# Optimization experiments

Hardware: AMD Instinct MI355X
Metric: run time of the kernel (lower is better)

Reference implementation:

```python
import jax, jax.numpy as jnp
import numpy as np

K = 9          # kernel_size
CENTER = K // 2
EXTEND = 1.0   # extend_scope
B, C_IN, C_OUT, H, W = 2, 64, 64, 256, 256


def group_norm(x, w, b, groups, eps=1e-5):
    Bx, C, Hx, Wx = x.shape
    xg = x.reshape(Bx, groups, C // groups, Hx, Wx)
    m = xg.mean(axis=(2, 3, 4), keepdims=True)
    v = xg.var(axis=(2, 3, 4), keepdims=True)
    xn = ((xg - m) * jax.lax.rsqrt(v + eps)).reshape(Bx, C, Hx, Wx)
    return xn * w[None, :, None, None] + b[None, :, None, None]


def conv2d(x, w, b, stride, padding):
    y = jax.lax.conv_general_dilated(x, w, stride, padding,
                                     dimension_numbers=('NCHW', 'OIHW', 'NCHW'))
    return y + b[None, :, None, None]


def bilinear_sample(feat, iy, ix):
    # feat [B,C,H,W]; iy/ix pixel coords [B,Hg,Wg]; align_corners=True bilinear
    Hf, Wf = feat.shape[2], feat.shape[3]
    y0 = jnp.floor(iy); x0 = jnp.floor(ix)
    wy1 = iy - y0; wx1 = ix - x0
    wy0 = 1.0 - wy1; wx0 = 1.0 - wx1
    y0i = jnp.clip(y0, 0, Hf - 1).astype(jnp.int32)
    y1i = jnp.clip(y0 + 1, 0, Hf - 1).astype(jnp.int32)
    x0i = jnp.clip(x0, 0, Wf - 1).astype(jnp.int32)
    x1i = jnp.clip(x0 + 1, 0, Wf - 1).astype(jnp.int32)
    g = jax.vmap(lambda f, yi, xi: f[:, yi, xi])  # per-batch gather -> [B,C,Hg,Wg]
    return (g(feat, y0i, x0i) * (wy0 * wx0)[:, None]
            + g(feat, y0i, x1i) * (wy0 * wx1)[:, None]
            + g(feat, y1i, x0i) * (wy1 * wx0)[:, None]
            + g(feat, y1i, x1i) * (wy1 * wx1)[:, None])


def outward_cumsum(off):
    # off [B,K,H,W]: center row -> 0, cumulative sums outward from center
    lower = jnp.flip(jnp.cumsum(jnp.flip(off[:, :CENTER], axis=1), axis=1), axis=1)
    upper = jnp.cumsum(off[:, CENTER + 1:], axis=1)
    zero = jnp.zeros_like(off[:, :1])
    return jnp.concatenate([lower, zero, upper], axis=1)


def reference(x, w_off, b_off, gno_w, gno_b, w_dsc, b_dsc, gn_w, gn_b):
    Bx, _, Hx, Wx = x.shape
    # offset branch: conv3x3 -> GroupNorm(K, 2K) -> tanh
    offset = conv2d(x, w_off, b_off, (1, 1), ((1, 1), (1, 1)))
    offset = jnp.tanh(group_norm(offset, gno_w, gno_b, groups=K))
    y_off = offset[:, :K]                      # morph=0 uses the y half
    y_cum = outward_cumsum(y_off)              # [B,K,H,W]
    y_center = jnp.arange(Hx, dtype=x.dtype)[None, None, :, None]
    x_base = (jnp.arange(Wx, dtype=x.dtype)[None, None, None, :]
              + jnp.linspace(-CENTER, CENTER, K, dtype=x.dtype)[None, :, None, None])
    y_new = y_center + EXTEND * y_cum          # [B,K,H,W]
    x_new = jnp.broadcast_to(x_base, y_new.shape)
    # permute(0,2,1,3).reshape -> [B, K*H, W]
    ycoord = y_new.transpose(0, 2, 1, 3).reshape(Bx, Hx * K, Wx)
    xcoord = x_new.transpose(0, 2, 1, 3).reshape(Bx, Hx * K, Wx)
    # clamp to [0,max] then [-1,1] normalize + align_corners unnormalize == clamp
    iy = jnp.clip(ycoord, 0.0, Hx - 1.0)
    ix = jnp.clip(xcoord, 0.0, Wx - 1.0)
    deformed = bilinear_sample(x, iy, ix)      # [B,C,K*H,W]
    out = conv2d(deformed, w_dsc, b_dsc, (K, 1), 'VALID')  # [B,Cout,H,W]
    out = group_norm(out, gn_w, gn_b, groups=C_OUT // 4)
    return jax.nn.relu(out)


def setup_inputs() -> dict:
    key = jax.random.key(0)
    ks = jax.random.split(key, 3)
    return {
        'x': jax.random.normal(ks[0], (B, C_IN, H, W), dtype=jnp.float32),
        'w_off': jax.random.normal(ks[1], (2 * K, C_IN, 3, 3), dtype=jnp.float32) * 0.05,
        'b_off': jnp.zeros((2 * K,), dtype=jnp.float32),
        'gno_w': jnp.ones((2 * K,), dtype=jnp.float32),
        'gno_b': jnp.zeros((2 * K,), dtype=jnp.float32),
        'w_dsc': jax.random.normal(ks[2], (C_OUT, C_IN, K, 1), dtype=jnp.float32) * 0.05,
        'b_dsc': jnp.zeros((C_OUT,), dtype=jnp.float32),
        'gn_w': jnp.ones((C_OUT,), dtype=jnp.float32),
        'gn_b': jnp.zeros((C_OUT,), dtype=jnp.float32),
    }
```

## Files before the change

### kernel.cpp

```cpp
#include <hip/hip_runtime.h>
#include <hip/hip_fp16.h>
#include <math.h>

#define BB 2
#define CC 64
#define HH 256
#define WW 256
#define KK 9
#define NOFF 10
#define HW (HH*WW)

typedef __attribute__((ext_vector_type(8))) short s16x8;
typedef __attribute__((ext_vector_type(4))) float f32x4;

__device__ __forceinline__ unsigned lerp2h(unsigned a, unsigned b, __half2 fy2) {
    __half2 ah = *(__half2*)&a, bh = *(__half2*)&b;
    __half2 d = __hfma2(fy2, __hsub2(bh, ah), ah);
    return *(unsigned*)&d;
}

__global__ __launch_bounds__(256) void transpose_x_kernel(const float* __restrict__ x,
                                                          unsigned short* __restrict__ xTh) {
    __shared__ float tile[64 * 65];
    int wt = blockIdx.x & 3;
    int h  = (blockIdx.x >> 2) & 255;
    int b  = blockIdx.x >> 10;
    int w0 = wt * 64;
    int t  = threadIdx.x;
    {
        int wl = t & 63, crow = t >> 6;
        for (int it = 0; it < 16; ++it) {
            int c = crow + it * 4;
            tile[wl * 65 + c] = x[(((b * CC + c) * HH + h) * WW) + w0 + wl];
        }
    }
    __syncthreads();
    {
        int c2 = t & 31, wrow = t >> 5;
        unsigned* dst = (unsigned*)xTh;
        for (int it = 0; it < 8; ++it) {
            int wl = wrow + it * 8;
            __half2 p = __floats2half2_rn(tile[wl * 65 + c2 * 2], tile[wl * 65 + c2 * 2 + 1]);
            dst[(((b * HH + h) * WW) + w0 + wl) * 32 + c2] = *(unsigned*)&p;
        }
    }
}

__global__ __launch_bounds__(256) void pack_weights_kernel(const float* __restrict__ w_off,
                                                           const float* __restrict__ w_dsc,
                                                           unsigned short* __restrict__ woffB,
                                                           unsigned short* __restrict__ wdscB) {
    int idx = blockIdx.x * 256 + threadIdx.x;
    if (idx < 18 * 64 * 8) {
        int kb = idx >> 9;
        int L  = (idx >> 3) & 63;
        int j  = idx & 7;
        int n = L & 15, quad = L >> 4;
        int kk = kb * 32 + quad * 8 + j;
        int tap = kk >> 6, ci = kk & 63;
        float v = (n < NOFF) ? w_off[(n * 64 + ci) * 9 + tap] : 0.f;
        __half hv = __float2half(v);
        woffB[idx] = *(unsigned short*)&hv;
    }
    if (idx < 4 * 18 * 64 * 8) {
        int nt = idx / 9216;
        int r  = idx - nt * 9216;
        int kb = r >> 9;
        int L  = (r >> 3) & 63;
        int j  = r & 7;
        int n = L & 15, quad = L >> 4;
        int co = nt * 16 + n;
        int kk = kb * 32 + quad * 8 + j;
        int k = kk >> 6, ci = kk & 63;
        __half hv = __float2half(w_dsc[(co * 64 + ci) * 9 + k]);
        wdscB[idx] = *(unsigned short*)&hv;
    }
}

#define CPITCH 72
__global__ __launch_bounds__(256, 4) void conv_off_mfma(const unsigned short* __restrict__ xTh,
                                                        const unsigned short* __restrict__ woffB,
                                                        const float* __restrict__ b_off,
                                                        float* __restrict__ off_raw,
                                                        float* __restrict__ partials_off) {
    __shared__ unsigned short sx[3 * 66 * CPITCH];
    __shared__ float rs[4][16], rs2[4][16];
    int t = threadIdx.x;
    int L = t & 63, v = t >> 6;
    int b  = blockIdx.x >> 10;
    int h  = (blockIdx.x >> 2) & 255;
    int w0 = (blockIdx.x & 3) << 6;
    int col = L & 15, quad = L >> 4;

#pragma unroll
    for (int it = 0; it < 7; ++it) {
        int linear = it * 256 + t;
        if (linear < 1584) {
            int dy  = linear / 528;
            int rem = linear - dy * 528;
            int px  = rem >> 3, cg = rem & 7;
            int y  = h - 1 + dy;
            int xc = w0 - 1 + px;
            uint4 d = make_uint4(0, 0, 0, 0);
            if ((unsigned)y < 256u && (unsigned)xc < 256u)
                d = *(const uint4*)(xTh + ((size_t)(((b << 8) + y) << 8) + xc) * 64 + cg * 8);
            *(uint4*)&sx[(dy * 66 + px) * CPITCH + cg * 8] = d;
        }
    }

    s16x8 breg[18];
#pragma unroll
    for (int kb = 0; kb < 18; ++kb)
        breg[kb] = *(const s16x8*)(woffB + (kb * 64 + L) * 8);
    __syncthreads();

    f32x4 acc = {0.f, 0.f, 0.f, 0.f};
#pragma unroll
    for (int kb = 0; kb < 18; ++kb) {
        int tap = kb >> 1;
        int dy = tap / 3, dxl = tap % 3;
        int pxl = v * 16 + col + dxl;
        int ci0 = ((kb & 1) << 5) + quad * 8;
        s16x8 a = *(const s16x8*)&sx[(dy * 66 + pxl) * CPITCH + ci0];
        acc = __builtin_amdgcn_mfma_f32_16x16x32_f16(a, breg[kb], acc, 0, 0, 0);
    }
    int oc = col;
    float bo = b_off[oc];
    float s = 0.f, s2 = 0.f;
#pragma unroll
    for (int r = 0; r < 4; ++r) {
        float val = acc[r] + bo;
        if (oc < NOFF) {
            int w = w0 + v * 16 + quad * 4 + r;
            off_raw[((b * NOFF + oc) << 16) + (h << 8) + w] = val;
        }
        s += val; s2 += val * val;
    }
    s  += __shfl_xor(s, 16, 64);  s  += __shfl_xor(s, 32, 64);
    s2 += __shfl_xor(s2, 16, 64); s2 += __shfl_xor(s2, 32, 64);
    if (quad == 0) { rs[v][oc] = s; rs2[v][oc] = s2; }
    __syncthreads();
    if (t < NOFF) {
        float a_ = rs[0][t] + rs[1][t] + rs[2][t] + rs[3][t];
        float a2 = rs2[0][t] + rs2[1][t] + rs2[2][t] + rs2[3][t];
        partials_off[(size_t)blockIdx.x * 20 + t * 2]     = a_;
        partials_off[(size_t)blockIdx.x * 20 + t * 2 + 1] = a2;
    }
}

__global__ __launch_bounds__(256) void reduce_off_kernel(const float* __restrict__ partials,
                                                         float* __restrict__ stats) {
    int bg = blockIdx.x;
    int b = bg / 5, g = bg - b * 5;
    int t = threadIdx.x;
    float s = 0.f, s2 = 0.f;
    for (int i = t; i < 1024; i += 256) {
        const float* p = partials + ((size_t)(b * 1024 + i)) * 20 + g * 4;
        s  += p[0] + p[2];
        s2 += p[1] + p[3];
    }
    __shared__ float rs[256], rs2[256];
    rs[t] = s; rs2[t] = s2;
    __syncthreads();
    for (int o = 128; o > 0; o >>= 1) {
        if (t < o) { rs[t] += rs[t + o]; rs2[t] += rs2[t + o]; }
        __syncthreads();
    }
    if (t == 0) {
        float mean = rs[0] * (1.f / 131072.f);
        float var  = rs2[0] * (1.f / 131072.f) - mean * mean;
        stats[bg * 2]     = mean;
        stats[bg * 2 + 1] = rsqrtf(var + 1e-5f);
    }
}

__global__ __launch_bounds__(256) void reduce_out_kernel(const float* __restrict__ partials,
                                                         float* __restrict__ stats) {
    int bg = blockIdx.x;
    int b = bg >> 4, g = bg & 15;
    int t = threadIdx.x;
    float s = 0.f, s2 = 0.f;
    for (int i = t; i < 1024; i += 256) {
        const float* p = partials + ((size_t)(b * 1024 + i)) * 32 + g * 2;
        s  += p[0];
        s2 += p[1];
    }
    __shared__ float rs[256], rs2[256];
    rs[t] = s; rs2[t] = s2;
    __syncthreads();
    for (int o = 128; o > 0; o >>= 1) {
        if (t < o) { rs[t] += rs[t + o]; rs2[t] += rs2[t + o]; }
        __syncthreads();
    }
    if (t == 0) {
        float mean = rs[0] * (1.f / 262144.f);
        float var  = rs2[0] * (1.f / 262144.f) - mean * mean;
        stats[bg * 2]     = mean;
        stats[bg * 2 + 1] = rsqrtf(var + 1e-5f);
    }
}

__global__ __launch_bounds__(256, 4) void main_mfma(const unsigned short* __restrict__ xTh,
                                                    const float* __restrict__ off_raw,
                                                    const float* __restrict__ stats_off,
                                                    const float* __restrict__ gno_w,
                                                    const float* __restrict__ gno_b,
                                                    const unsigned short* __restrict__ wdscB,
                                                    const float* __restrict__ b_dsc,
                                                    unsigned short* __restrict__ tmph,
                                                    float* __restrict__ partials_out) {
    __shared__ unsigned short aT[32 * 584];
    __shared__ int            offA0[576];
    __shared__ unsigned short fyH[576];

    int t = threadIdx.x;
    int L = t & 63, nt = t >> 6;
    int b  = blockIdx.x >> 10;
    int h  = (blockIdx.x >> 2) & 255;
    int w0 = (blockIdx.x & 3) << 6;

    if (t < 64) {
        int w = w0 + t;
        float tk[9];
#pragma unroll
        for (int k = 0; k < 9; ++k) {
            float vv = off_raw[((b * NOFF + k) << 16) + (h << 8) + w];
            int g = k >> 1;
            float mean = stats_off[(b * 5 + g) * 2];
            float rstd = stats_off[(b * 5 + g) * 2 + 1];
            tk[k] = tanhf((vv - mean) * rstd * gno_w[k] + gno_b[k]);
        }
        float yc[9];
        float c = 0.f;
#pragma unroll
        for (int k = 3; k >= 0; --k) { c += tk[k]; yc[k] = c; }
        yc[4] = 0.f;
        c = 0.f;
#pragma unroll
        for (int k = 5; k < 9; ++k) { c += tk[k]; yc[k] = c; }
#pragma unroll
        for (int k = 0; k < 9; ++k) {
            float y = fminf(fmaxf((float)h + yc[k], 0.f), 255.f);
            float y0f = floorf(y);
            int y0 = (int)y0f;
            int xc = min(max(w + k - 4, 0), 255);
            offA0[t * 9 + k] = ((b * 256 + y0) * 256 + xc) * 64;
            __half fh = __float2half(y - y0f);
            fyH[t * 9 + k] = *(unsigned short*)&fh;
        }
    }

    s16x8 wreg[18];
#pragma unroll
    for (int kb = 0; kb < 18; ++kb)
        wreg[kb] = *(const s16x8*)(wdscB + ((nt * 18 + kb) * 64 + L) * 8);

    int col = L & 15, quad = L >> 4;
    int co = nt * 16 + col;
    float bias = b_dsc[co];
    float ss = 0.f, ss2 = 0.f;

    for (int round = 0; round < 2; ++round) {
        __syncthreads();
#pragma unroll
        for (int it = 0; it < 9; ++it) {
            int idx = it * 256 + t;
            int cg  = idx & 7;
            int r2  = idx >> 3;
            int pxl = r2 / 9;
            int k   = r2 - pxl * 9;
            int pi  = (round * 32 + pxl) * 9 + k;
            int o0 = offA0[pi] + cg * 8;
            unsigned short fb = fyH[pi];
            int o1 = fb ? o0 + 16384 : o0;
            __half fh = *(__half*)&fb;
            __half2 fy2 = __half2half2(fh);
            uint4 u0 = *(const uint4*)(xTh + o0);
            uint4 u1 = *(const uint4*)(xTh + o1);
            uint4 d;
            d.x = lerp2h(u0.x, u1.x, fy2);
            d.y = lerp2h(u0.y, u1.y, fy2);
            d.z = lerp2h(u0.z, u1.z, fy2);
            d.w = lerp2h(u0.w, u1.w, fy2);
            int c2 = (cg + k) & 7;
            *(uint4*)&aT[pxl * 584 + k * 64 + c2 * 8] = d;
        }
        __syncthreads();

#pragma unroll
        for (int sub = 0; sub < 2; ++sub) {
            int row = sub * 16 + col;
            f32x4 acc = {0.f, 0.f, 0.f, 0.f};
#pragma unroll
            for (int kb = 0; kb < 18; ++kb) {
                int k  = kb >> 1;
                int cch = ((kb & 1) << 2) + quad;
                int c2 = (cch + k) & 7;
                s16x8 a = *(const s16x8*)&aT[row * 584 + k * 64 + c2 * 8];
                acc = __builtin_amdgcn_mfma_f32_16x16x32_f16(a, wreg[kb], acc, 0, 0, 0);
            }
            int wbase = w0 + round * 32 + sub * 16 + quad * 4;
            size_t obase = ((size_t)((b << 16) + (h << 8) + wbase)) * 64 + co;
#pragma unroll
            for (int r = 0; r < 4; ++r) {
                float val = acc[r] + bias;
                ss += val; ss2 += val * val;
                __half hv = __float2half(val);
                tmph[obase + (size_t)r * 64] = *(unsigned short*)&hv;
            }
        }
    }
    ss  += __shfl_xor(ss, 16, 64);  ss  += __shfl_xor(ss, 32, 64);
    ss2 += __shfl_xor(ss2, 16, 64); ss2 += __shfl_xor(ss2, 32, 64);
    float sg = ss, sg2 = ss2;
    sg  += __shfl_xor(sg, 1, 64);  sg  += __shfl_xor(sg, 2, 64);
    sg2 += __shfl_xor(sg2, 1, 64); sg2 += __shfl_xor(sg2, 2, 64);
    if (quad == 0 && (col & 3) == 0) {
        int gi = nt * 4 + (col >> 2);
        partials_out[(size_t)blockIdx.x * 32 + gi * 2]     = sg;
        partials_out[(size_t)blockIdx.x * 32 + gi * 2 + 1] = sg2;
    }
}

__global__ __launch_bounds__(256) void apply_final_kernel(const unsigned short* __restrict__ tmph,
                                                          const float* __restrict__ stats_out,
                                                          const float* __restrict__ gn_w,
                                                          const float* __restrict__ gn_b,
                                                          float* __restrict__ out) {
    __shared__ float tile[64 * 65];
    int wt = blockIdx.x & 3;
    int h  = (blockIdx.x >> 2) & 255;
    int b  = blockIdx.x >> 10;
    int w0 = wt * 64;
    int t  = threadIdx.x;
    {
        int c2 = t & 31, wrow = t >> 5;
        int co0 = c2 * 2;
        int g = co0 >> 2;
        float mean = stats_out[(b * 16 + g) * 2];
        float rstd = stats_out[(b * 16 + g) * 2 + 1];
        float sc0 = rstd * gn_w[co0],     sh0 = gn_b[co0]     - mean * sc0;
        float sc1 = rstd * gn_w[co0 + 1], sh1 = gn_b[co0 + 1] - mean * sc1;
        const unsigned* src = (const unsigned*)tmph;
        for (int it = 0; it < 8; ++it) {
            int wl = wrow + it * 8;
            unsigned u = src[(((b * HH + h) * WW) + w0 + wl) * 32 + c2];
            float2 f = __half22float2(*(__half2*)&u);
            tile[co0 * 65 + wl]       = fmaxf(fmaf(f.x, sc0, sh0), 0.f);
            tile[(co0 + 1) * 65 + wl] = fmaxf(fmaf(f.y, sc1, sh1), 0.f);
        }
    }
    __syncthreads();
    {
        int wl = t & 63, crow = t >> 6;
        for (int it = 0; it < 16; ++it) {
            int co = crow + it * 4;
            out[((size_t)(b * CC + co) * HH + h) * WW + w0 + wl] = tile[co * 65 + wl];
        }
    }
}

extern "C" void kernel_launch(void* const* d_in, const int* in_sizes, int n_in,
                              void* d_out, int out_size, void* d_ws, size_t ws_size,
                              hipStream_t stream) {
    const float* x     = (const float*)d_in[0];
    const float* w_off = (const float*)d_in[1];
    const float* b_off = (const float*)d_in[2];
    const float* gno_w = (const float*)d_in[3];
    const float* gno_b = (const float*)d_in[4];
    const float* w_dsc = (const float*)d_in[5];
    const float* b_dsc = (const float*)d_in[6];
    const float* gn_w  = (const float*)d_in[7];
    const float* gn_b  = (const float*)d_in[8];
    float* out = (float*)d_out;

    char* ws = (char*)d_ws;
    unsigned short* xTh   = (unsigned short*)(ws);
    unsigned short* tmph  = (unsigned short*)(ws + 16777216);
    float* off_raw        = (float*)(ws + 33554432);
    unsigned short* wdscB = (unsigned short*)(ws + 38797312);
    unsigned short* woffB = (unsigned short*)(ws + 38871040);
    float* stats_off      = (float*)(ws + 38889472);
    float* stats_out      = (float*)(ws + 38889728);
    float* partials_off   = (float*)(ws + 38890496);
    float* partials_out   = (float*)(ws + 39054336);

    hipLaunchKernelGGL(transpose_x_kernel, dim3(2048), dim3(256), 0, stream, x, xTh);
    hipLaunchKernelGGL(pack_weights_kernel, dim3(144), dim3(256), 0, stream,
                       w_off, w_dsc, woffB, wdscB);
    hipLaunchKernelGGL(conv_off_mfma, dim3(2048), dim3(256), 0, stream,
                       xTh, woffB, b_off, off_raw, partials_off);
    hipLaunchKernelGGL(reduce_off_kernel, dim3(10), dim3(256), 0, stream,
                       partials_off, stats_off);
    hipLaunchKernelGGL(main_mfma, dim3(2048), dim3(256), 0, stream,
                       xTh, off_raw, stats_off, gno_w, gno_b, wdscB, b_dsc,
                       tmph, partials_out);
    hipLaunchKernelGGL(reduce_out_kernel, dim3(32), dim3(256), 0, stream,
                       partials_out, stats_out);
    hipLaunchKernelGGL(apply_final_kernel, dim3(2048), dim3(256), 0, stream,
                       tmph, stats_out, gn_w, gn_b, out);
}
```

Baseline: 163.7 us.

## Merge weight packing into transpose, shrink main tile, parallelize offset tanh

Folds the weight-packing kernel into the transpose kernel as extra blocks, removing one launch. In main_mfma, the LDS A-tile is halved (16 pixels per round, 4 rounds) and launch bounds are raised to 6 waves/EU to increase occupancy. The tanh/GroupNorm offset computation is spread across all 256 threads via a shared buffer instead of only 64 threads. The weight register loads are moved ahead of the barrier to overlap with it. The cost is more barriers per block and possible register pressure under the tighter launch bound.

```diff
diff --git a/kernel.cpp b/kernel.cpp
--- a/kernel.cpp
+++ b/kernel.cpp
@@ -20,7 +20,39 @@
 }
 
 __global__ __launch_bounds__(256) void transpose_x_kernel(const float* __restrict__ x,
-                                                          unsigned short* __restrict__ xTh) {
+                                                          unsigned short* __restrict__ xTh,
+                                                          const float* __restrict__ w_off,
+                                                          const float* __restrict__ w_dsc,
+                                                          unsigned short* __restrict__ woffB,
+                                                          unsigned short* __restrict__ wdscB) {
+    if (blockIdx.x >= 2048) {
+        int idx = (blockIdx.x - 2048) * 256 + threadIdx.x;
+        if (idx < 18 * 64 * 8) {
+            int kb = idx >> 9;
+            int L  = (idx >> 3) & 63;
+            int j  = idx & 7;
+            int n = L & 15, quad = L >> 4;
+            int kk = kb * 32 + quad * 8 + j;
+            int tap = kk >> 6, ci = kk & 63;
+            float v = (n < NOFF) ? w_off[(n * 64 + ci) * 9 + tap] : 0.f;
+            __half hv = __float2half(v);
+            woffB[idx] = *(unsigned short*)&hv;
+        }
+        if (idx < 4 * 18 * 64 * 8) {
+            int nt = idx / 9216;
+            int r  = idx - nt * 9216;
+            int kb = r >> 9;
+            int L  = (r >> 3) & 63;
+            int j  = r & 7;
+            int n = L & 15, quad = L >> 4;
+            int co = nt * 16 + n;
+            int kk = kb * 32 + quad * 8 + j;
+            int k = kk >> 6, ci = kk & 63;
+            __half hv = __float2half(w_dsc[(co * 64 + ci) * 9 + k]);
+            wdscB[idx] = *(unsigned short*)&hv;
+        }
+        return;
+    }
     __shared__ float tile[64 * 65];
     int wt = blockIdx.x & 3;
     int h  = (blockIdx.x >> 2) & 255;
@@ -43,37 +75,6 @@
             __half2 p = __floats2half2_rn(tile[wl * 65 + c2 * 2], tile[wl * 65 + c2 * 2 + 1]);
             dst[(((b * HH + h) * WW) + w0 + wl) * 32 + c2] = *(unsigned*)&p;
         }
-    }
-}
-
-__global__ __launch_bounds__(256) void pack_weights_kernel(const float* __restrict__ w_off,
-                                                           const float* __restrict__ w_dsc,
-                                                           unsigned short* __restrict__ woffB,
-                                                           unsigned short* __restrict__ wdscB) {
-    int idx = blockIdx.x * 256 + threadIdx.x;
-    if (idx < 18 * 64 * 8) {
-        int kb = idx >> 9;
-        int L  = (idx >> 3) & 63;
-        int j  = idx & 7;
-        int n = L & 15, quad = L >> 4;
-        int kk = kb * 32 + quad * 8 + j;
-        int tap = kk >> 6, ci = kk & 63;
-        float v = (n < NOFF) ? w_off[(n * 64 + ci) * 9 + tap] : 0.f;
-        __half hv = __float2half(v);
-        woffB[idx] = *(unsigned short*)&hv;
-    }
-    if (idx < 4 * 18 * 64 * 8) {
-        int nt = idx / 9216;
-        int r  = idx - nt * 9216;
-        int kb = r >> 9;
-        int L  = (r >> 3) & 63;
-        int j  = r & 7;
-        int n = L & 15, quad = L >> 4;
-        int co = nt * 16 + n;
-        int kk = kb * 32 + quad * 8 + j;
-        int k = kk >> 6, ci = kk & 63;
-        __half hv = __float2half(w_dsc[(co * 64 + ci) * 9 + k]);
-        wdscB[idx] = *(unsigned short*)&hv;
     }
 }
 
@@ -200,7 +201,7 @@
     }
 }
 
-__global__ __launch_bounds__(256, 4) void main_mfma(const unsigned short* __restrict__ xTh,
+__global__ __launch_bounds__(256, 6) void main_mfma(const unsigned short* __restrict__ xTh,
                                                     const float* __restrict__ off_raw,
                                                     const float* __restrict__ stats_off,
                                                     const float* __restrict__ gno_w,
@@ -209,9 +210,10 @@
                                                     const float* __restrict__ b_dsc,
                                                     unsigned short* __restrict__ tmph,
                                                     float* __restrict__ partials_out) {
-    __shared__ unsigned short aT[32 * 584];
+    __shared__ unsigned short aT[16 * 584];
     __shared__ int            offA0[576];
     __shared__ unsigned short fyH[576];
+    __shared__ float          tkL[576];
 
     int t = threadIdx.x;
     int L = t & 63, nt = t >> 6;
@@ -219,17 +221,27 @@
     int h  = (blockIdx.x >> 2) & 255;
     int w0 = (blockIdx.x & 3) << 6;
 
+    for (int i = t; i < 576; i += 256) {
+        int k = i >> 6, w = i & 63;
+        float vv = off_raw[((b * NOFF + k) << 16) + (h << 8) + w0 + w];
+        int g = k >> 1;
+        float mean = stats_off[(b * 5 + g) * 2];
+        float rstd = stats_off[(b * 5 + g) * 2 + 1];
+        tkL[w * 9 + k] = tanhf((vv - mean) * rstd * gno_w[k] + gno_b[k]);
+    }
+
+    s16x8 wreg[18];
+#pragma unroll
+    for (int kb = 0; kb < 18; ++kb)
+        wreg[kb] = *(const s16x8*)(wdscB + ((nt * 18 + kb) * 64 + L) * 8);
+
+    __syncthreads();
+
     if (t < 64) {
         int w = w0 + t;
         float tk[9];
 #pragma unroll
-        for (int k = 0; k < 9; ++k) {
-            float vv = off_raw[((b * NOFF + k) << 16) + (h << 8) + w];
-            int g = k >> 1;
-            float mean = stats_off[(b * 5 + g) * 2];
-            float rstd = stats_off[(b * 5 + g) * 2 + 1];
-            tk[k] = tanhf((vv - mean) * rstd * gno_w[k] + gno_b[k]);
-        }
+        for (int k = 0; k < 9; ++k) tk[k] = tkL[t * 9 + k];
         float yc[9];
         float c = 0.f;
 #pragma unroll
@@ -250,26 +262,19 @@
         }
     }
 
-    s16x8 wreg[18];
-#pragma unroll
-    for (int kb = 0; kb < 18; ++kb)
-        wreg[kb] = *(const s16x8*)(wdscB + ((nt * 18 + kb) * 64 + L) * 8);
-
     int col = L & 15, quad = L >> 4;
     int co = nt * 16 + col;
     float bias = b_dsc[co];
     float ss = 0.f, ss2 = 0.f;
 
-    for (int round = 0; round < 2; ++round) {
+    for (int round = 0; round < 4; ++round) {
         __syncthreads();
-#pragma unroll
-        for (int it = 0; it < 9; ++it) {
-            int idx = it * 256 + t;
+        for (int idx = t; idx < 1152; idx += 256) {
             int cg  = idx & 7;
             int r2  = idx >> 3;
             int pxl = r2 / 9;
             int k   = r2 - pxl * 9;
-            int pi  = (round * 32 + pxl) * 9 + k;
+            int pi  = (round * 16 + pxl) * 9 + k;
             int o0 = offA0[pi] + cg * 8;
             unsigned short fb = fyH[pi];
             int o1 = fb ? o0 + 16384 : o0;
@@ -287,27 +292,23 @@
         }
         __syncthreads();
 
-#pragma unroll
-        for (int sub = 0; sub < 2; ++sub) {
-            int row = sub * 16 + col;
-            f32x4 acc = {0.f, 0.f, 0.f, 0.f};
-#pragma unroll
-            for (int kb = 0; kb < 18; ++kb) {
-                int k  = kb >> 1;
-                int cch = ((kb & 1) << 2) + quad;
-                int c2 = (cch + k) & 7;
-                s16x8 a = *(const s16x8*)&aT[row * 584 + k * 64 + c2 * 8];
-                acc = __builtin_amdgcn_mfma_f32_16x16x32_f16(a, wreg[kb], acc, 0, 0, 0);
-            }
-            int wbase = w0 + round * 32 + sub * 16 + quad * 4;
-            size_t obase = ((size_t)((b << 16) + (h << 8) + wbase)) * 64 + co;
-#pragma unroll
-            for (int r = 0; r < 4; ++r) {
-                float val = acc[r] + bias;
-                ss += val; ss2 += val * val;
-                __half hv = __float2half(val);
-                tmph[obase + (size_t)r * 64] = *(unsigned short*)&hv;
-            }
+        f32x4 acc = {0.f, 0.f, 0.f, 0.f};
+#pragma unroll
+        for (int kb = 0; kb < 18; ++kb) {
+            int k  = kb >> 1;
+            int cch = ((kb & 1) << 2) + quad;
+            int c2 = (cch + k) & 7;
+            s16x8 a = *(const s16x8*)&aT[col * 584 + k * 64 + c2 * 8];
+            acc = __builtin_amdgcn_mfma_f32_16x16x32_f16(a, wreg[kb], acc, 0, 0, 0);
+        }
+        int wbase = w0 + round * 16 + quad * 4;
+        size_t obase = ((size_t)((b << 16) + (h << 8) + wbase)) * 64 + co;
+#pragma unroll
+        for (int r = 0; r < 4; ++r) {
+            float val = acc[r] + bias;
+            ss += val; ss2 += val * val;
+            __half hv = __float2half(val);
+            tmph[obase + (size_t)r * 64] = *(unsigned short*)&hv;
         }
     }
     ss  += __shfl_xor(ss, 16, 64);  ss  += __shfl_xor(ss, 32, 64);
@@ -385,9 +386,8 @@
     float* partials_off   = (float*)(ws + 38890496);
     float* partials_out   = (float*)(ws + 39054336);
 
-    hipLaunchKernelGGL(transpose_x_kernel, dim3(2048), dim3(256), 0, stream, x, xTh);
-    hipLaunchKernelGGL(pack_weights_kernel, dim3(144), dim3(256), 0, stream,
-                       w_off, w_dsc, woffB, wdscB);
+    hipLaunchKernelGGL(transpose_x_kernel, dim3(2192), dim3(256), 0, stream,
+                       x, xTh, w_off, w_dsc, woffB, wdscB);
     hipLaunchKernelGGL(conv_off_mfma, dim3(2048), dim3(256), 0, stream,
                        xTh, woffB, b_off, off_raw, partials_off);
     hipLaunchKernelGGL(reduce_off_kernel, dim3(10), dim3(256), 0, stream,
```

Measured after the change: 192.0 us. 17.3% more time.

## Fuse weight packing into transpose, store offsets in fp16, swizzle blocks across XCDs

Applied to the files above, without the earlier changes.

Weight packing now runs as extra blocks of the transpose kernel, which saves one kernel launch. The raw offset-conv outputs are stored as fp16 instead of fp32, halving that intermediate's traffic. Block indices in conv_off and main_mfma are remapped so consecutive rows land on the same XCD for better L2 locality, and the reduce kernels invert that mapping when summing partials. main_mfma also packs y0, x and the fraction into one 32-bit shared-memory word. The fp16 rounding of offsets adds precision risk to the sampling coordinates.

```diff
diff --git a/kernel.cpp b/kernel.cpp
--- a/kernel.cpp
+++ b/kernel.cpp
@@ -19,8 +19,48 @@
     return *(unsigned*)&d;
 }
 
+__device__ __forceinline__ void swizzle_bhw(int g, int& b, int& h, int& wt) {
+    int W = ((g & 7) << 8) | (g >> 3);
+    b  = W >> 10;
+    int rem = W & 1023;
+    h  = rem >> 2;
+    wt = rem & 3;
+}
+
 __global__ __launch_bounds__(256) void transpose_x_kernel(const float* __restrict__ x,
-                                                          unsigned short* __restrict__ xTh) {
+                                                          unsigned short* __restrict__ xTh,
+                                                          const float* __restrict__ w_off,
+                                                          const float* __restrict__ w_dsc,
+                                                          unsigned short* __restrict__ woffB,
+                                                          unsigned short* __restrict__ wdscB) {
+    if (blockIdx.x >= 2048) {
+        int idx = (blockIdx.x - 2048) * 256 + threadIdx.x;
+        if (idx < 18 * 64 * 8) {
+            int kb = idx >> 9;
+            int L  = (idx >> 3) & 63;
+            int j  = idx & 7;
+            int n = L & 15, quad = L >> 4;
+            int kk = kb * 32 + quad * 8 + j;
+            int tap = kk >> 6, ci = kk & 63;
+            float v = (n < NOFF) ? w_off[(n * 64 + ci) * 9 + tap] : 0.f;
+            __half hv = __float2half(v);
+            woffB[idx] = *(unsigned short*)&hv;
+        }
+        if (idx < 4 * 18 * 64 * 8) {
+            int nt = idx / 9216;
+            int r  = idx - nt * 9216;
+            int kb = r >> 9;
+            int L  = (r >> 3) & 63;
+            int j  = r & 7;
+            int n = L & 15, quad = L >> 4;
+            int co = nt * 16 + n;
+            int kk = kb * 32 + quad * 8 + j;
+            int k = kk >> 6, ci = kk & 63;
+            __half hv = __float2half(w_dsc[(co * 64 + ci) * 9 + k]);
+            wdscB[idx] = *(unsigned short*)&hv;
+        }
+        return;
+    }
     __shared__ float tile[64 * 65];
     int wt = blockIdx.x & 3;
     int h  = (blockIdx.x >> 2) & 255;
@@ -46,50 +86,19 @@
     }
 }
 
-__global__ __launch_bounds__(256) void pack_weights_kernel(const float* __restrict__ w_off,
-                                                           const float* __restrict__ w_dsc,
-                                                           unsigned short* __restrict__ woffB,
-                                                           unsigned short* __restrict__ wdscB) {
-    int idx = blockIdx.x * 256 + threadIdx.x;
-    if (idx < 18 * 64 * 8) {
-        int kb = idx >> 9;
-        int L  = (idx >> 3) & 63;
-        int j  = idx & 7;
-        int n = L & 15, quad = L >> 4;
-        int kk = kb * 32 + quad * 8 + j;
-        int tap = kk >> 6, ci = kk & 63;
-        float v = (n < NOFF) ? w_off[(n * 64 + ci) * 9 + tap] : 0.f;
-        __half hv = __float2half(v);
-        woffB[idx] = *(unsigned short*)&hv;
-    }
-    if (idx < 4 * 18 * 64 * 8) {
-        int nt = idx / 9216;
-        int r  = idx - nt * 9216;
-        int kb = r >> 9;
-        int L  = (r >> 3) & 63;
-        int j  = r & 7;
-        int n = L & 15, quad = L >> 4;
-        int co = nt * 16 + n;
-        int kk = kb * 32 + quad * 8 + j;
-        int k = kk >> 6, ci = kk & 63;
-        __half hv = __float2half(w_dsc[(co * 64 + ci) * 9 + k]);
-        wdscB[idx] = *(unsigned short*)&hv;
-    }
-}
-
 #define CPITCH 72
 __global__ __launch_bounds__(256, 4) void conv_off_mfma(const unsigned short* __restrict__ xTh,
                                                         const unsigned short* __restrict__ woffB,
                                                         const float* __restrict__ b_off,
-                                                        float* __restrict__ off_raw,
+                                                        unsigned short* __restrict__ off_raw,
                                                         float* __restrict__ partials_off) {
     __shared__ unsigned short sx[3 * 66 * CPITCH];
     __shared__ float rs[4][16], rs2[4][16];
     int t = threadIdx.x;
     int L = t & 63, v = t >> 6;
-    int b  = blockIdx.x >> 10;
-    int h  = (blockIdx.x >> 2) & 255;
-    int w0 = (blockIdx.x & 3) << 6;
+    int b, h, wt;
+    swizzle_bhw(blockIdx.x, b, h, wt);
+    int w0 = wt << 6;
     int col = L & 15, quad = L >> 4;
 
 #pragma unroll
@@ -132,7 +141,8 @@
         float val = acc[r] + bo;
         if (oc < NOFF) {
             int w = w0 + v * 16 + quad * 4 + r;
-            off_raw[((b * NOFF + oc) << 16) + (h << 8) + w] = val;
+            __half hv = __float2half(val);
+            off_raw[((b * NOFF + oc) << 16) + (h << 8) + w] = *(unsigned short*)&hv;
         }
         s += val; s2 += val * val;
     }
@@ -151,13 +161,16 @@
 __global__ __launch_bounds__(256) void reduce_off_kernel(const float* __restrict__ partials,
                                                          float* __restrict__ stats) {
     int bg = blockIdx.x;
-    int b = bg / 5, g = bg - b * 5;
     int t = threadIdx.x;
     float s = 0.f, s2 = 0.f;
-    for (int i = t; i < 1024; i += 256) {
-        const float* p = partials + ((size_t)(b * 1024 + i)) * 20 + g * 4;
-        s  += p[0] + p[2];
-        s2 += p[1] + p[3];
+    int b = bg / 5, gg = bg - b * 5;
+    for (int i = t; i < 2048; i += 256) {
+        int blk_b = (((i & 7) << 8) | (i >> 3)) >> 10;
+        if (blk_b == b) {
+            const float* p = partials + (size_t)i * 20 + gg * 4;
+            s  += p[0] + p[2];
+            s2 += p[1] + p[3];
+        }
     }
     __shared__ float rs[256], rs2[256];
     rs[t] = s; rs2[t] = s2;
@@ -180,10 +193,13 @@
     int b = bg >> 4, g = bg & 15;
     int t = threadIdx.x;
     float s = 0.f, s2 = 0.f;
-    for (int i = t; i < 1024; i += 256) {
-        const float* p = partials + ((size_t)(b * 1024 + i)) * 32 + g * 2;
-        s  += p[0];
-        s2 += p[1];
+    for (int i = t; i < 2048; i += 256) {
+        int blk_b = (((i & 7) << 8) | (i >> 3)) >> 10;
+        if (blk_b == b) {
+            const float* p = partials + (size_t)i * 32 + g * 2;
+            s  += p[0];
+            s2 += p[1];
+        }
     }
     __shared__ float rs[256], rs2[256];
     rs[t] = s; rs2[t] = s2;
@@ -201,7 +217,7 @@
 }
 
 __global__ __launch_bounds__(256, 4) void main_mfma(const unsigned short* __restrict__ xTh,
-                                                    const float* __restrict__ off_raw,
+                                                    const unsigned short* __restrict__ off_raw,
                                                     const float* __restrict__ stats_off,
                                                     const float* __restrict__ gno_w,
                                                     const float* __restrict__ gno_b,
@@ -210,21 +226,21 @@
                                                     unsigned short* __restrict__ tmph,
                                                     float* __restrict__ partials_out) {
     __shared__ unsigned short aT[32 * 584];
-    __shared__ int            offA0[576];
-    __shared__ unsigned short fyH[576];
+    __shared__ unsigned       coordA[576];
 
     int t = threadIdx.x;
     int L = t & 63, nt = t >> 6;
-    int b  = blockIdx.x >> 10;
-    int h  = (blockIdx.x >> 2) & 255;
-    int w0 = (blockIdx.x & 3) << 6;
+    int b, h, wt;
+    swizzle_bhw(blockIdx.x, b, h, wt);
+    int w0 = wt << 6;
 
     if (t < 64) {
         int w = w0 + t;
         float tk[9];
 #pragma unroll
         for (int k = 0; k < 9; ++k) {
-            float vv = off_raw[((b * NOFF + k) << 16) + (h << 8) + w];
+            unsigned short u = off_raw[((b * NOFF + k) << 16) + (h << 8) + w];
+            float vv = __half2float(*(__half*)&u);
             int g = k >> 1;
             float mean = stats_off[(b * 5 + g) * 2];
             float rstd = stats_off[(b * 5 + g) * 2 + 1];
@@ -244,9 +260,9 @@
             float y0f = floorf(y);
             int y0 = (int)y0f;
             int xc = min(max(w + k - 4, 0), 255);
-            offA0[t * 9 + k] = ((b * 256 + y0) * 256 + xc) * 64;
             __half fh = __float2half(y - y0f);
-            fyH[t * 9 + k] = *(unsigned short*)&fh;
+            coordA[t * 9 + k] = (unsigned)y0 | ((unsigned)xc << 8)
+                              | ((unsigned)(*(unsigned short*)&fh) << 16);
         }
     }
 
@@ -259,6 +275,7 @@
     int co = nt * 16 + col;
     float bias = b_dsc[co];
     float ss = 0.f, ss2 = 0.f;
+    int bBase = b << 22;
 
     for (int round = 0; round < 2; ++round) {
         __syncthreads();
@@ -270,8 +287,9 @@
             int pxl = r2 / 9;
             int k   = r2 - pxl * 9;
             int pi  = (round * 32 + pxl) * 9 + k;
-            int o0 = offA0[pi] + cg * 8;
-            unsigned short fb = fyH[pi];
+            unsigned pc = coordA[pi];
+            int o0 = bBase + ((pc & 255) << 14) + (((pc >> 8) & 255) << 6) + cg * 8;
+            unsigned short fb = (unsigned short)(pc >> 16);
             int o1 = fb ? o0 + 16384 : o0;
             __half fh = *(__half*)&fb;
             __half2 fy2 = __half2half2(fh);
@@ -375,19 +393,18 @@
     float* out = (float*)d_out;
 
     char* ws = (char*)d_ws;
-    unsigned short* xTh   = (unsigned short*)(ws);
-    unsigned short* tmph  = (unsigned short*)(ws + 16777216);
-    float* off_raw        = (float*)(ws + 33554432);
-    unsigned short* wdscB = (unsigned short*)(ws + 38797312);
-    unsigned short* woffB = (unsigned short*)(ws + 38871040);
-    float* stats_off      = (float*)(ws + 38889472);
-    float* stats_out      = (float*)(ws + 38889728);
-    float* partials_off   = (float*)(ws + 38890496);
-    float* partials_out   = (float*)(ws + 39054336);
-
-    hipLaunchKernelGGL(transpose_x_kernel, dim3(2048), dim3(256), 0, stream, x, xTh);
-    hipLaunchKernelGGL(pack_weights_kernel, dim3(144), dim3(256), 0, stream,
-                       w_off, w_dsc, woffB, wdscB);
+    unsigned short* xTh     = (unsigned short*)(ws);
+    unsigned short* tmph    = (unsigned short*)(ws + 16777216);
+    unsigned short* off_raw = (unsigned short*)(ws + 33554432);
+    unsigned short* wdscB   = (unsigned short*)(ws + 36175872);
+    unsigned short* woffB   = (unsigned short*)(ws + 36249600);
+    float* stats_off        = (float*)(ws + 36268032);
+    float* stats_out        = (float*)(ws + 36268288);
+    float* partials_off     = (float*)(ws + 36268544);
+    float* partials_out     = (float*)(ws + 36432384);
+
+    hipLaunchKernelGGL(transpose_x_kernel, dim3(2192), dim3(256), 0, stream,
+                       x, xTh, w_off, w_dsc, woffB, wdscB);
     hipLaunchKernelGGL(conv_off_mfma, dim3(2048), dim3(256), 0, stream,
                        xTh, woffB, b_off, off_raw, partials_off);
     hipLaunchKernelGGL(reduce_off_kernel, dim3(10), dim3(256), 0, stream,
```

New measurement: 156.7 us. -4.3%, faster.
